# Performance work log

Measured on AMD Instinct MI355X. Metric: run time of the kernel, lower is better.

The kernel has to match this reference:

```python
import jax, jax.numpy as jnp
import numpy as np

B, S, IN, D, H, L, DFF, NT, K = 32, 512, 256, 512, 8, 2, 2048, 424, 25
DK = D // H


def moving_avg_trend(x, k):
    # AvgPool1d(kernel=k, stride=1, pad=k//2, count_include_pad=False) along seq axis
    b, s, d = x.shape
    half = k // 2
    cs = jnp.cumsum(x, axis=1)
    cs = jnp.concatenate([jnp.zeros((b, 1, d), x.dtype), cs], axis=1)  # [b, s+1, d]
    idx = jnp.arange(s)
    hi = jnp.minimum(idx + half + 1, s)
    lo = jnp.maximum(idx - half, 0)
    win = cs[:, hi] - cs[:, lo]                    # windowed sums [b, s, d]
    cnt = (hi - lo).astype(x.dtype)
    return win / cnt[None, :, None]


def auto_correlation(x, qkvo_w, qkvo_b):
    b, s, d = x.shape
    Q = (x @ qkvo_w[0] + qkvo_b[0]).reshape(b, s, H, DK)
    Kt = (x @ qkvo_w[1] + qkvo_b[1]).reshape(b, s, H, DK)
    V = (x @ qkvo_w[2] + qkvo_b[2]).reshape(b, s, H, DK)
    Qf = jnp.fft.rfft(Q, axis=1)
    Kf = jnp.fft.rfft(Kt, axis=1)
    corr = jnp.fft.irfft(Qf * jnp.conj(Kf), n=s, axis=1)
    corr = jax.nn.softmax(corr, axis=1)
    out = (corr * V).reshape(b, s, d)
    return out @ qkvo_w[3] + qkvo_b[3]


def encoder_layer(x, qkvo_w, qkvo_b, w1, b1, w2, b2):
    x_corr = auto_correlation(x, qkvo_w, qkvo_b)
    y = x + x_corr
    x = y - moving_avg_trend(y, K)                 # seasonal component (decomp1)
    ffn = jax.nn.gelu(x @ w1 + b1) @ w2 + b2
    y = x + ffn
    x = y - moving_avg_trend(y, K)                 # decomp2
    return x


def setup_inputs() -> dict:
    key = jax.random.key(0)
    ks = jax.random.split(key, 16)
    sc = 0.02
    return {
        "x": jax.random.normal(ks[0], (B, S, IN), jnp.float32),
        "embed_w": jax.random.normal(ks[1], (IN, D), jnp.float32) * sc,
        "embed_b": jnp.zeros((D,), jnp.float32),
        "qkvo_w": jax.random.normal(ks[2], (L, 4, D, D), jnp.float32) * sc,
        "qkvo_b": jnp.zeros((L, 4, D), jnp.float32),
        "ffn_w1": jax.random.normal(ks[3], (L, D, DFF), jnp.float32) * sc,
        "ffn_b1": jnp.zeros((L, DFF), jnp.float32),
        "ffn_w2": jax.random.normal(ks[4], (L, DFF, D), jnp.float32) * sc,
        "ffn_b2": jnp.zeros((L, D), jnp.float32),
        "proj_w1": jax.random.normal(ks[5], (D, D // 2), jnp.float32) * sc,
        "proj_b1": jnp.zeros((D // 2,), jnp.float32),
        "proj_w2": jax.random.normal(ks[6], (D // 2, NT), jnp.float32) * sc,
        "proj_b2": jnp.zeros((NT,), jnp.float32),
    }


def reference(x, embed_w, embed_b, qkvo_w, qkvo_b, ffn_w1, ffn_b1, ffn_w2, ffn_b2,
              proj_w1, proj_b1, proj_w2, proj_b2):
    h = x @ embed_w + embed_b
    for l in range(L):
        h = encoder_layer(h, qkvo_w[l], qkvo_b[l], ffn_w1[l], ffn_b1[l], ffn_w2[l], ffn_b2[l])
    h = h.mean(axis=1)                             # [B, D]
    h = jax.nn.relu(h @ proj_w1 + proj_b1)
    return h @ proj_w2 + proj_b2                   # [B, NT]
```

## Files before the change

### kernel.cpp

```cpp
#include <hip/hip_runtime.h>
#include <hip/hip_bf16.h>

#define S_LEN 512
#define D_DIM 512
#define B_DIM 32
#define IN_DIM 256
#define DFF_DIM 2048
#define NT_DIM 424

static constexpr size_t SZ = (size_t)B_DIM * S_LEN * D_DIM;

using s8v = __attribute__((ext_vector_type(8))) short;
using f4v = __attribute__((ext_vector_type(4))) float;
typedef unsigned short ushortT;

__device__ __forceinline__ ushortT f2bf(float f) {
  unsigned u = __float_as_uint(f);
  u += 0x7FFFu + ((u >> 16) & 1u);
  return (ushortT)(u >> 16);
}

__device__ __forceinline__ float gelu_tanh(float x) {
  float x3 = x * x * x;
  return 0.5f * x * (1.f + tanhf(0.7978845608028654f * (x + 0.044715f * x3)));
}

__device__ __forceinline__ float2 cadd(float2 a, float2 b) { return float2{a.x + b.x, a.y + b.y}; }
__device__ __forceinline__ float2 csub(float2 a, float2 b) { return float2{a.x - b.x, a.y - b.y}; }
__device__ __forceinline__ float2 cmul(float2 a, float2 b) {
  return float2{a.x * b.x - a.y * b.y, a.x * b.y + a.y * b.x};
}
__device__ __forceinline__ float2 mni(float2 a) { return float2{a.y, -a.x}; }

__device__ __forceinline__ void dft8(float2 a[8]) {
  float2 t0 = cadd(a[0], a[4]), t4 = csub(a[0], a[4]);
  float2 t1 = cadd(a[1], a[5]), t5 = csub(a[1], a[5]);
  float2 t2 = cadd(a[2], a[6]), t6 = csub(a[2], a[6]);
  float2 t3 = cadd(a[3], a[7]), t7 = csub(a[3], a[7]);
  float2 u0 = cadd(t0, t2), u2 = csub(t0, t2);
  float2 u1 = cadd(t1, t3), u3 = csub(t1, t3);
  const float C = 0.70710678118654752f;
  float2 s5 = float2{C * (t5.x + t5.y), C * (t5.y - t5.x)};
  float2 s6 = mni(t6);
  float2 s7 = float2{C * (t7.y - t7.x), -C * (t7.x + t7.y)};
  float2 v0 = cadd(t4, s6), v2 = csub(t4, s6);
  float2 v1 = cadd(s5, s7), v3 = csub(s5, s7);
  a[0] = cadd(u0, u1); a[4] = csub(u0, u1);
  a[2] = cadd(u2, mni(u3)); a[6] = csub(u2, mni(u3));
  a[1] = cadd(v0, v1); a[5] = csub(v0, v1);
  a[3] = cadd(v2, mni(v3)); a[7] = csub(v2, mni(v3));
}

__global__ __launch_bounds__(256) void conv_all(
    const float* __restrict__ embed_w, const float* __restrict__ qkvo_w,
    const float* __restrict__ ffn_w1, const float* __restrict__ ffn_w2,
    ushortT* __restrict__ embed_wt, ushortT* __restrict__ qkvo_wt,
    ushortT* __restrict__ ffn1_wt, ushortT* __restrict__ ffn2_wt)
{
  __shared__ float T[32][33];
  const int z = blockIdx.z;
  const float* W; ushortT* Wt; int Kp, N;
  if (z == 0)       { W = embed_w; Wt = embed_wt; Kp = 256; N = 512; }
  else if (z <= 8)  { int i = z - 1; W = qkvo_w + (size_t)i * 512 * 512;
                      Wt = qkvo_wt + (size_t)i * 512 * 512; Kp = 512; N = 512; }
  else if (z <= 10) { int l = z - 9; W = ffn_w1 + (size_t)l * 512 * 2048;
                      Wt = ffn1_wt + (size_t)l * 2048 * 512; Kp = 512; N = 2048; }
  else              { int l = z - 11; W = ffn_w2 + (size_t)l * 2048 * 512;
                      Wt = ffn2_wt + (size_t)l * 512 * 2048; Kp = 2048; N = 512; }
  int k0, n0;
  if (z >= 11) { k0 = blockIdx.y * 32; n0 = blockIdx.x * 32; }
  else         { k0 = blockIdx.x * 32; n0 = blockIdx.y * 32; }
  if (k0 >= Kp || n0 >= N) return;

  const int tid = threadIdx.x;
  const int col = tid & 31, r8 = tid >> 5;
#pragma unroll
  for (int it = 0; it < 4; ++it) {
    int row = r8 + it * 8;
    T[row][col] = W[(size_t)(k0 + row) * N + n0 + col];
  }
  __syncthreads();
  const int nl = tid >> 3, kq = tid & 7;
#pragma unroll
  for (int j = 0; j < 4; ++j) {
    int kl = kq * 4 + j;
    Wt[(size_t)(n0 + nl) * Kp + k0 + kl] = f2bf(T[kl][nl]);
  }
}

__global__ __launch_bounds__(256) void cvt_bf16(
    const float* __restrict__ in, ushortT* __restrict__ out, int n4)
{
  int i = blockIdx.x * 256 + threadIdx.x;
  if (i >= n4) return;
  float4 v = ((const float4*)in)[i];
  ushortT o[4] = {f2bf(v.x), f2bf(v.y), f2bf(v.z), f2bf(v.w)};
  *(uint2*)&out[(size_t)i * 4] = *(const uint2*)o;
}

template<int ACT, int RES, int OUT>
__global__ __launch_bounds__(256) void gemm_bf16(
    const ushortT* __restrict__ A, const ushortT* __restrict__ Wt,
    const float* __restrict__ bias, const float* __restrict__ res,
    float* __restrict__ C, ushortT* __restrict__ Cb,
    ushortT* __restrict__ Qh, ushortT* __restrict__ Kh, int M, int Kp, int N)
{
  __shared__ ushortT Ash[2][128 * 32];
  __shared__ ushortT Wsh[2][128 * 32];
  const int tid = threadIdx.x;
  const int lane = tid & 63, wid = tid >> 6;
  const int fr = lane & 15, kq = lane >> 4;
  const int wr = wid >> 1, wc = wid & 1;

  const int nwg = gridDim.x * gridDim.y;
  const int bid = blockIdx.y * gridDim.x + blockIdx.x;
  const int swz = (bid & 7) * (nwg >> 3) + (bid >> 3);
  const int bx = swz % gridDim.x, by = swz / gridDim.x;
  const int m0 = by * 128, n0 = bx * 128;

  int srow[2], skq[2];
#pragma unroll
  for (int t = 0; t < 2; ++t) {
    int ch = wid * 2 + t;
    int row = ch * 16 + (lane >> 2);
    int kql = lane & 3;
    srow[t] = row;
    skq[t] = kql ^ ((row >> 1) & 3);
  }

  int aoff[4], boff[4];
#pragma unroll
  for (int i = 0; i < 4; ++i) {
    int ra = wr * 64 + i * 16 + fr;
    aoff[i] = ra * 32 + ((kq ^ ((ra >> 1) & 3)) << 3);
    int rb = wc * 64 + i * 16 + fr;
    boff[i] = rb * 32 + ((kq ^ ((rb >> 1) & 3)) << 3);
  }

  auto STAGE = [&](int buf, int k0) {
#pragma unroll
    for (int t = 0; t < 2; ++t) {
      const ushortT* as = A + (size_t)(m0 + srow[t]) * Kp + k0 + skq[t] * 8;
      __builtin_amdgcn_global_load_lds(
          (const __attribute__((address_space(1))) unsigned int*)as,
          (__attribute__((address_space(3))) unsigned int*)&Ash[buf][(wid * 2 + t) * 512],
          16, 0, 0);
      const ushortT* wsrc = Wt + (size_t)(n0 + srow[t]) * Kp + k0 + skq[t] * 8;
      __builtin_amdgcn_global_load_lds(
          (const __attribute__((address_space(1))) unsigned int*)wsrc,
          (__attribute__((address_space(3))) unsigned int*)&Wsh[buf][(wid * 2 + t) * 512],
          16, 0, 0);
    }
  };

  f4v acc[4][4] = {};
  STAGE(0, 0);
  int cur = 0;

  for (int k0 = 0; k0 < Kp; k0 += 32) {
    __syncthreads();
    if (k0 + 32 < Kp) STAGE(cur ^ 1, k0 + 32);
    s8v af[4], bfv[4];
#pragma unroll
    for (int i = 0; i < 4; ++i) {
      af[i]  = *(const s8v*)&Ash[cur][aoff[i]];
      bfv[i] = *(const s8v*)&Wsh[cur][boff[i]];
    }
#pragma unroll
    for (int i = 0; i < 4; ++i)
#pragma unroll
      for (int j = 0; j < 4; ++j)
        acc[i][j] = __builtin_amdgcn_mfma_f32_16x16x32_bf16(af[i], bfv[j], acc[i][j], 0, 0, 0);
    cur ^= 1;
  }

#pragma unroll
  for (int j = 0; j < 4; ++j) {
    const int gc = n0 + wc * 64 + j * 16 + fr;
    const float bv = bias[gc];
#pragma unroll
    for (int i = 0; i < 4; ++i) {
      const int gr0 = m0 + wr * 64 + i * 16 + kq * 4;
      if (OUT == 3) {
        if (gc < 1024) {
          ushortT h4[4];
#pragma unroll
          for (int r = 0; r < 4; ++r) {
            _Float16 hh = (_Float16)(acc[i][j][r] + bv);
            h4[r] = __builtin_bit_cast(ushortT, hh);
          }
          ushortT* dst = (gc < 512 ? Qh : Kh)
                       + ((size_t)(gr0 >> 9) * 512 + (gc & 511)) * 512 + (gr0 & 511);
          *(uint2*)dst = *(const uint2*)h4;
        } else {
#pragma unroll
          for (int r = 0; r < 4; ++r)
            C[(size_t)(gr0 + r) * D_DIM + (gc & 511)] = acc[i][j][r] + bv;
        }
      } else {
#pragma unroll
        for (int r = 0; r < 4; ++r) {
          const int gr = gr0 + r;
          float v = acc[i][j][r] + bv;
          if (RES) v += res[(size_t)gr * N + gc];
          if (ACT == 1) v = gelu_tanh(v);
          if (OUT != 2) C[(size_t)gr * N + gc] = v;
          if (OUT != 0) Cb[(size_t)gr * N + gc] = f2bf(v);
        }
      }
    }
  }
}

__global__ __launch_bounds__(512) void autocorr_fft(
    const ushortT* __restrict__ Qh, const ushortT* __restrict__ Kh,
    const float* __restrict__ V, ushortT* __restrict__ Ob)
{
  __shared__ float2 zs[8 * 578];
  const int tid = threadIdx.x;
  const int b  = blockIdx.x >> 6;
  const int c0 = (blockIdx.x & 63) << 3;
  const int ch = tid >> 6;
  const int t  = tid & 63;
  float2* zc = &zs[ch * 578];

  {
    const ushortT* Qg = Qh + ((size_t)b * 512 + c0 + ch) * 512 + t * 8;
    const ushortT* Kg = Kh + ((size_t)b * 512 + c0 + ch) * 512 + t * 8;
    uint4 qv = *(const uint4*)Qg;
    uint4 kv = *(const uint4*)Kg;
    const ushortT* qp = (const ushortT*)&qv;
    const ushortT* kp = (const ushortT*)&kv;
    const int base = 9 * t;
#pragma unroll
    for (int j = 0; j < 8; ++j) {
      zc[base + j] = float2{(float)__builtin_bit_cast(_Float16, qp[j]),
                            (float)__builtin_bit_cast(_Float16, kp[j])};
    }
  }
  __syncthreads();

  float2 a[8];
  auto stage_fn = [&](int stage, bool do_scatter) {
#pragma unroll
    for (int r = 0; r < 8; ++r) { int ci = t + 64 * r; a[r] = zc[ci + (ci >> 3)]; }
    dft8(a);
    if (stage < 2) {
      float angle = (stage == 0) ? (-6.283185307179586f / 512.f) * (float)t
                                 : (-6.283185307179586f / 64.f) * (float)(t >> 3);
      float sn, cs;
      __sincosf(angle, &sn, &cs);
      float2 w = float2{cs, sn}, wp = w;
      a[1] = cmul(a[1], wp);
#pragma unroll
      for (int r = 2; r < 8; ++r) { wp = cmul(wp, w); a[r] = cmul(a[r], wp); }
    }
    if (!do_scatter) return;
    __syncthreads();
#pragma unroll
    for (int r = 0; r < 8; ++r) {
      int ci = (stage == 0) ? 8 * t + r
             : (stage == 1) ? (t & 7) + 64 * (t >> 3) + 8 * r
                            : t + 64 * r;
      zc[ci + (ci >> 3)] = a[r];
    }
    __syncthreads();
  };

  stage_fn(0, true); stage_fn(1, true); stage_fn(2, true);

  float2 Zk[8], Zm[8];
#pragma unroll
  for (int r = 0; r < 8; ++r) {
    int k = t + 64 * r, mk = (512 - k) & 511;
    Zk[r] = zc[k + (k >> 3)];
    Zm[r] = zc[mk + (mk >> 3)];
  }
  __syncthreads();
  const float S = 0.00048828125f;
#pragma unroll
  for (int r = 0; r < 8; ++r) {
    int k = t + 64 * r;
    float x1 = Zk[r].x, y1 = Zk[r].y, x2 = Zm[r].x, y2 = Zm[r].y;
    float sx = x1 + x2, dx = x1 - x2, sy = y1 + y2, dy = y1 - y2;
    float pre = sx * sy - dy * dx;
    float pim = sx * dx + dy * sy;
    zc[k + (k >> 3)] = float2{pre * S, -pim * S};
  }
  __syncthreads();

  stage_fn(0, true); stage_fn(1, true); stage_fn(2, false);

  float corr[8];
#pragma unroll
  for (int r = 0; r < 8; ++r) corr[r] = a[r].x;
  float mx = corr[0];
#pragma unroll
  for (int r = 1; r < 8; ++r) mx = fmaxf(mx, corr[r]);
#pragma unroll
  for (int o = 1; o < 64; o <<= 1) mx = fmaxf(mx, __shfl_xor(mx, o));
  float ex[8], sum = 0.f;
#pragma unroll
  for (int r = 0; r < 8; ++r) { ex[r] = __expf(corr[r] - mx); sum += ex[r]; }
#pragma unroll
  for (int o = 1; o < 64; o <<= 1) sum += __shfl_xor(sum, o);
  const float inv = 1.f / sum;

  __syncthreads();
  float* wl = (float*)zc;
#pragma unroll
  for (int r = 0; r < 8; ++r) wl[t + 64 * r] = ex[r] * inv;
  __syncthreads();

  const float* wall = (const float*)zs;
  const size_t base = (size_t)b * S_LEN * D_DIM + c0;
  for (int i = tid; i < 4096; i += 512) {
    int s = i >> 3, cc = i & 7;
    float wv = wall[cc * 1156 + s];
    size_t ad = base + (size_t)s * D_DIM + cc;
    Ob[ad] = f2bf(wv * V[ad]);
  }
}

template<int MEAN>
__global__ __launch_bounds__(256) void movavg_sub2(
    const float* __restrict__ y, float* __restrict__ outf,
    ushortT* __restrict__ outb, float* __restrict__ hm)
{
  __shared__ float ys[512 * 32];
  const int tid = threadIdx.x;
  const int b = blockIdx.y, d0 = blockIdx.x * 32;
  const float* yb = y + (size_t)b * S_LEN * D_DIM + d0;

#pragma unroll 4
  for (int p = 0; p < 16; ++p) {
    int i = p * 256 + tid;
    int s = i >> 3, dq = i & 7;
    float4 v = *(const float4*)(yb + (size_t)s * D_DIM + dq * 4);
    *(float4*)&ys[s * 32 + dq * 4] = v;
  }
  __syncthreads();

  const int d = tid & 31, sg = tid >> 5;
  const int s0 = sg * 64;
  int lo = max(s0 - 12, 0), hi = min(s0 + 13, S_LEN);
  float sum = 0.f;
  for (int t = lo; t < hi; ++t) sum += ys[t * 32 + d];

  float msum = 0.f;
  const size_t gb = (size_t)b * S_LEN * D_DIM + d0 + d;
  for (int i = 0; i < 64; ++i) {
    const int s = s0 + i;
    float val = ys[s * 32 + d] - sum / (float)(hi - lo);
    size_t g = gb + (size_t)s * D_DIM;
    outf[g] = val;
    outb[g] = f2bf(val);
    if (MEAN) msum += val;
    int add = s + 13;
    if (add < S_LEN) { sum += ys[add * 32 + d]; hi = add + 1; }
    int rem = s - 12;
    if (rem >= 0) { sum -= ys[rem * 32 + d]; lo = rem + 1; }
  }
  if (MEAN) atomicAdd(&hm[b * D_DIM + d0 + d], msum * (1.f / (float)S_LEN));
}

__global__ __launch_bounds__(256) void proj_head1(
    const float* __restrict__ hm, const float* __restrict__ W1,
    const float* __restrict__ b1, float* __restrict__ p1)
{
  __shared__ float hs[32 * 512];
  const int tid = threadIdx.x, n0 = blockIdx.x * 32;
  for (int i = tid; i < 16384; i += 256) hs[i] = hm[i];
  __syncthreads();
  const int n = tid & 31, mg = tid >> 5;
  float acc[4] = {};
  for (int k = 0; k < 512; ++k) {
    float w = W1[(size_t)k * 256 + n0 + n];
#pragma unroll
    for (int mi = 0; mi < 4; ++mi)
      acc[mi] = fmaf(hs[(mg * 4 + mi) * 512 + k], w, acc[mi]);
  }
  const float bb = b1[n0 + n];
#pragma unroll
  for (int mi = 0; mi < 4; ++mi)
    p1[(size_t)(mg * 4 + mi) * 256 + n0 + n] = fmaxf(acc[mi] + bb, 0.f);
}

__global__ __launch_bounds__(256) void proj_head2(
    const float* __restrict__ p1, const float* __restrict__ W2,
    const float* __restrict__ b2, float* __restrict__ out)
{
  __shared__ float ps[32 * 256];
  const int tid = threadIdx.x;
  for (int i = tid; i < 8192; i += 256) ps[i] = p1[i];
  __syncthreads();
  const int n = tid & 31, mg = tid >> 5;
  const int ng = blockIdx.x * 32 + n;
  const bool ok = ng < NT_DIM;
  float acc[4] = {};
  for (int k = 0; k < 256; ++k) {
    float w = ok ? W2[(size_t)k * NT_DIM + ng] : 0.f;
#pragma unroll
    for (int mi = 0; mi < 4; ++mi)
      acc[mi] = fmaf(ps[(mg * 4 + mi) * 256 + k], w, acc[mi]);
  }
  if (ok) {
    const float bb = b2[ng];
#pragma unroll
    for (int mi = 0; mi < 4; ++mi)
      out[(size_t)(mg * 4 + mi) * NT_DIM + ng] = acc[mi] + bb;
  }
}

extern "C" void kernel_launch(void* const* d_in, const int* in_sizes, int n_in,
                              void* d_out, int out_size, void* d_ws, size_t ws_size,
                              hipStream_t stream)
{
  const float* x       = (const float*)d_in[0];
  const float* embed_w = (const float*)d_in[1];
  const float* embed_b = (const float*)d_in[2];
  const float* qkvo_w  = (const float*)d_in[3];
  const float* qkvo_b  = (const float*)d_in[4];
  const float* ffn_w1  = (const float*)d_in[5];
  const float* ffn_b1  = (const float*)d_in[6];
  const float* ffn_w2  = (const float*)d_in[7];
  const float* ffn_b2  = (const float*)d_in[8];
  const float* proj_w1 = (const float*)d_in[9];
  const float* proj_b1 = (const float*)d_in[10];
  const float* proj_w2 = (const float*)d_in[11];
  const float* proj_b2 = (const float*)d_in[12];
  float* out = (float*)d_out;

  float* ws = (float*)d_ws;
  float* Bv = ws;
  float* Bh = ws + SZ;
  float* Bq = ws + 2 * SZ;
  float* Bk = ws + 3 * SZ;
  ushortT* Sb = (ushortT*)(ws + 4 * SZ);
  ushortT* Wb = (ushortT*)(ws + 4 * SZ + SZ / 2);
  ushortT* embed_wt = Wb;
  ushortT* qkvo_wt  = embed_wt + (size_t)512 * 256;
  ushortT* ffn1_wt  = qkvo_wt + (size_t)8 * 512 * 512;
  ushortT* ffn2_wt  = ffn1_wt + (size_t)2 * 2048 * 512;
  float* hm = (float*)(ffn2_wt + (size_t)2 * 512 * 2048);
  float* p1 = hm + 16384;
  ushortT* Hb  = (ushortT*)Bv;
  ushortT* xb  = (ushortT*)Bq;
  ushortT* QKh = (ushortT*)Bq;

  dim3 blk(256);

  hipMemsetAsync(hm, 0, 16384 * sizeof(float), stream);

  conv_all<<<dim3(16, 64, 13), blk, 0, stream>>>(
      embed_w, qkvo_w, ffn_w1, ffn_w2, embed_wt, qkvo_wt, ffn1_wt, ffn2_wt);

  cvt_bf16<<<dim3(4096), blk, 0, stream>>>(x, xb, B_DIM * S_LEN * IN_DIM / 4);

  gemm_bf16<0, 0, 1><<<dim3(4, 128), blk, 0, stream>>>(
      xb, embed_wt, embed_b, nullptr, Bh, Sb, nullptr, nullptr, 16384, IN_DIM, D_DIM);

  for (int l = 0; l < 2; ++l) {
    const ushortT* qw = qkvo_wt + (size_t)l * 4 * 512 * 512;
    const float* qb = qkvo_b + (size_t)l * 4 * 512;
    gemm_bf16<0, 0, 3><<<dim3(12, 128), blk, 0, stream>>>(
        Sb, qw, qb, nullptr, Bv, nullptr, QKh, QKh + SZ, 16384, 512, 1536);
    autocorr_fft<<<dim3(B_DIM * 64), dim3(512), 0, stream>>>(QKh, QKh + SZ, Bv, Sb);
    gemm_bf16<0, 1, 0><<<dim3(4, 128), blk, 0, stream>>>(
        Sb, qw + (size_t)3 * 512 * 512, qb + 1536, Bh, Bq, nullptr, nullptr, nullptr,
        16384, 512, 512);
    movavg_sub2<0><<<dim3(16, 32), blk, 0, stream>>>(Bq, Bk, Sb, nullptr);
    gemm_bf16<1, 0, 2><<<dim3(16, 128), blk, 0, stream>>>(
        Sb, ffn1_wt + (size_t)l * 2048 * 512, ffn_b1 + (size_t)l * DFF_DIM,
        nullptr, nullptr, Hb, nullptr, nullptr, 16384, 512, 2048);
    gemm_bf16<0, 1, 0><<<dim3(4, 128), blk, 0, stream>>>(
        Hb, ffn2_wt + (size_t)l * 512 * 2048, ffn_b2 + (size_t)l * D_DIM,
        Bk, Bq, nullptr, nullptr, nullptr, 16384, 2048, 512);
    if (l == 1)
      movavg_sub2<1><<<dim3(16, 32), blk, 0, stream>>>(Bq, Bh, Sb, hm);
    else
      movavg_sub2<0><<<dim3(16, 32), blk, 0, stream>>>(Bq, Bh, Sb, nullptr);
  }

  proj_head1<<<dim3(8), blk, 0, stream>>>(hm, proj_w1, proj_b1, p1);
  proj_head2<<<dim3(14), blk, 0, stream>>>(p1, proj_w2, proj_b2, out);
}
```

Before: 593.5 us.

## Stage GEMM epilogue through LDS for coalesced 16-byte stores; use exp-based GELU

The GEMM epilogue now writes results into shared memory reused from the operand buffers, then stores them as coalesced 16-byte vectors. This applies to the transposed fp16 Q/K output and to the bf16 output copies, replacing scattered 2-byte and 8-byte stores. GELU's tanh form is rewritten as x*sigmoid(2a) using __expf, which is cheaper. The cost is extra barriers and LDS traffic in the epilogue, plus slightly different GELU rounding.

New measurement: 556.7 us. 1.07x faster.

```diff
diff --git a/kernel.cpp b/kernel.cpp
--- a/kernel.cpp
+++ b/kernel.cpp
@@ -20,9 +20,9 @@
   return (ushortT)(u >> 16);
 }
 
-__device__ __forceinline__ float gelu_tanh(float x) {
-  float x3 = x * x * x;
-  return 0.5f * x * (1.f + tanhf(0.7978845608028654f * (x + 0.044715f * x3)));
+__device__ __forceinline__ float gelu_fast(float x) {
+  float a = 1.5957691216057308f * (x + 0.044715f * x * x * x);
+  return x / (1.f + __expf(-a));
 }
 
 __device__ __forceinline__ float2 cadd(float2 a, float2 b) { return float2{a.x + b.x, a.y + b.y}; }
@@ -105,8 +105,9 @@
     float* __restrict__ C, ushortT* __restrict__ Cb,
     ushortT* __restrict__ Qh, ushortT* __restrict__ Kh, int M, int Kp, int N)
 {
-  __shared__ ushortT Ash[2][128 * 32];
-  __shared__ ushortT Wsh[2][128 * 32];
+  __shared__ __align__(16) ushortT smem[16896];
+  ushortT* Tt = smem;
+
   const int tid = threadIdx.x;
   const int lane = tid & 63, wid = tid >> 6;
   const int fr = lane & 15, kq = lane >> 4;
@@ -143,12 +144,12 @@
       const ushortT* as = A + (size_t)(m0 + srow[t]) * Kp + k0 + skq[t] * 8;
       __builtin_amdgcn_global_load_lds(
           (const __attribute__((address_space(1))) unsigned int*)as,
-          (__attribute__((address_space(3))) unsigned int*)&Ash[buf][(wid * 2 + t) * 512],
+          (__attribute__((address_space(3))) unsigned int*)&smem[buf * 4096 + (wid * 2 + t) * 512],
           16, 0, 0);
       const ushortT* wsrc = Wt + (size_t)(n0 + srow[t]) * Kp + k0 + skq[t] * 8;
       __builtin_amdgcn_global_load_lds(
           (const __attribute__((address_space(1))) unsigned int*)wsrc,
-          (__attribute__((address_space(3))) unsigned int*)&Wsh[buf][(wid * 2 + t) * 512],
+          (__attribute__((address_space(3))) unsigned int*)&smem[8192 + buf * 4096 + (wid * 2 + t) * 512],
           16, 0, 0);
     }
   };
@@ -163,8 +164,8 @@
     s8v af[4], bfv[4];
 #pragma unroll
     for (int i = 0; i < 4; ++i) {
-      af[i]  = *(const s8v*)&Ash[cur][aoff[i]];
-      bfv[i] = *(const s8v*)&Wsh[cur][boff[i]];
+      af[i]  = *(const s8v*)&smem[cur * 4096 + aoff[i]];
+      bfv[i] = *(const s8v*)&smem[8192 + cur * 4096 + boff[i]];
     }
 #pragma unroll
     for (int i = 0; i < 4; ++i)
@@ -174,39 +175,73 @@
     cur ^= 1;
   }
 
-#pragma unroll
-  for (int j = 0; j < 4; ++j) {
-    const int gc = n0 + wc * 64 + j * 16 + fr;
-    const float bv = bias[gc];
-#pragma unroll
-    for (int i = 0; i < 4; ++i) {
-      const int gr0 = m0 + wr * 64 + i * 16 + kq * 4;
-      if (OUT == 3) {
-        if (gc < 1024) {
-          ushortT h4[4];
-#pragma unroll
-          for (int r = 0; r < 4; ++r) {
-            _Float16 hh = (_Float16)(acc[i][j][r] + bv);
-            h4[r] = __builtin_bit_cast(ushortT, hh);
-          }
-          ushortT* dst = (gc < 512 ? Qh : Kh)
-                       + ((size_t)(gr0 >> 9) * 512 + (gc & 511)) * 512 + (gr0 & 511);
-          *(uint2*)dst = *(const uint2*)h4;
-        } else {
-#pragma unroll
-          for (int r = 0; r < 4; ++r)
-            C[(size_t)(gr0 + r) * D_DIM + (gc & 511)] = acc[i][j][r] + bv;
+  if (OUT == 3 && n0 < 1024) {
+    __syncthreads();
+#pragma unroll
+    for (int j = 0; j < 4; ++j) {
+      const int c = wc * 64 + j * 16 + fr;
+      const float bv = bias[n0 + c];
+#pragma unroll
+      for (int i = 0; i < 4; ++i)
+#pragma unroll
+        for (int r = 0; r < 4; ++r) {
+          const int s = wr * 64 + i * 16 + kq * 4 + r;
+          _Float16 hh = (_Float16)(acc[i][j][r] + bv);
+          Tt[c * 132 + s] = __builtin_bit_cast(ushortT, hh);
         }
-      } else {
+    }
+    __syncthreads();
+    ushortT* dstM = (n0 < 512) ? Qh : Kh;
+    const int cg0 = n0 & 511;
+    const int bb = m0 >> 9, ss0 = m0 & 511;
+    const int g = tid >> 4, ln = tid & 15;
+#pragma unroll
+    for (int p = 0; p < 8; ++p) {
+      const int c = p * 16 + g;
+      uint4 v = *(const uint4*)&Tt[c * 132 + ln * 8];
+      *(uint4*)&dstM[((size_t)bb * 512 + cg0 + c) * 512 + ss0 + ln * 8] = v;
+    }
+  } else if (OUT == 3) {
+#pragma unroll
+    for (int j = 0; j < 4; ++j) {
+      const int gc = n0 + wc * 64 + j * 16 + fr;
+      const float bv = bias[gc];
+#pragma unroll
+      for (int i = 0; i < 4; ++i) {
+        const int gr0 = m0 + wr * 64 + i * 16 + kq * 4;
+#pragma unroll
+        for (int r = 0; r < 4; ++r)
+          C[(size_t)(gr0 + r) * D_DIM + (gc & 511)] = acc[i][j][r] + bv;
+      }
+    }
+  } else {
+    if (OUT != 0) __syncthreads();
+#pragma unroll
+    for (int j = 0; j < 4; ++j) {
+      const int lc = wc * 64 + j * 16 + fr;
+      const int gc = n0 + lc;
+      const float bv = bias[gc];
+#pragma unroll
+      for (int i = 0; i < 4; ++i)
 #pragma unroll
         for (int r = 0; r < 4; ++r) {
-          const int gr = gr0 + r;
+          const int lr = wr * 64 + i * 16 + kq * 4 + r;
+          const int gr = m0 + lr;
           float v = acc[i][j][r] + bv;
           if (RES) v += res[(size_t)gr * N + gc];
-          if (ACT == 1) v = gelu_tanh(v);
+          if (ACT == 1) v = gelu_fast(v);
           if (OUT != 2) C[(size_t)gr * N + gc] = v;
-          if (OUT != 0) Cb[(size_t)gr * N + gc] = f2bf(v);
+          if (OUT != 0) Tt[lr * 132 + lc] = f2bf(v);
         }
+    }
+    if (OUT != 0) {
+      __syncthreads();
+      const int g = tid >> 4, ln = tid & 15;
+#pragma unroll
+      for (int p = 0; p < 8; ++p) {
+        const int row = p * 16 + g;
+        uint4 v = *(const uint4*)&Tt[row * 132 + ln * 8];
+        *(uint4*)&Cb[(size_t)(m0 + row) * N + n0 + ln * 8] = v;
       }
     }
   }
```
